# Performance work log

Measured on AMD Instinct MI355X. Metric: run time of the kernel, lower is better.

Reference implementation:

```python
import jax, jax.numpy as jnp
import numpy as np

HIDDEN_DIM = 64
VOCAB_SIZE = 128
NUM_SLOTS = 64
B, L = 256, 4096


def layer_norm(x, gamma, beta, eps=1e-5):
    mu = jnp.mean(x, axis=-1, keepdims=True)
    var = jnp.mean(jnp.square(x - mu), axis=-1, keepdims=True)
    return (x - mu) * jax.lax.rsqrt(var + eps) * gamma + beta


def _l2norm(x, axis=-1, eps=1e-12):
    # matches torch F.normalize: x / max(||x||, eps)
    n = jnp.sqrt(jnp.sum(jnp.square(x), axis=axis, keepdims=True))
    return x / jnp.maximum(n, eps)


def setup_inputs() -> dict:
    key = jax.random.key(0)
    ks = jax.random.split(key, 13)
    H, V, S = HIDDEN_DIM, VOCAB_SIZE, NUM_SLOTS
    return {
        "seq": jax.random.randint(ks[0], (B, L), 0, V),
        "embed_w": jax.random.normal(ks[1], (V, H), dtype=jnp.float32),
        # linear weights stored [in, out] (transposed vs torch)
        "w1": jax.random.normal(ks[2], (H, 2 * H), dtype=jnp.float32) * 0.05,
        "b1": jnp.zeros((2 * H,), dtype=jnp.float32),
        "w2": jax.random.normal(ks[3], (2 * H, H), dtype=jnp.float32) * 0.05,
        "b2": jnp.zeros((H,), dtype=jnp.float32),
        "ln_g": jnp.ones((H,), dtype=jnp.float32),
        "ln_b": jnp.zeros((H,), dtype=jnp.float32),
        "slot_keys": jax.random.normal(ks[4], (S, H), dtype=jnp.float32) * 0.1,
        "slot_vals": jax.random.normal(ks[5], (S, H), dtype=jnp.float32) * 0.1,
        "gate_w": jax.random.normal(ks[6], (H, S), dtype=jnp.float32) * 0.05,
        "gate_b": jnp.zeros((S,), dtype=jnp.float32),
        "out_w": jax.random.normal(ks[7], (H, V), dtype=jnp.float32) * 0.05,
        "out_b": jnp.zeros((V,), dtype=jnp.float32),
    }


def reference(seq, embed_w, w1, b1, w2, b2, ln_g, ln_b,
              slot_keys, slot_vals, gate_w, gate_b, out_w, out_b):
    h = embed_w[seq]                                   # [B, L, H]
    ff = jnp.maximum(h @ w1 + b1, 0.0) @ w2 + b2       # [B, L, H]
    h = layer_norm(h + ff, ln_g, ln_b)

    hw = h[:, :-1, :]                                  # written tokens [B, L-1, H]
    w = jax.nn.softmax(hw @ gate_w + gate_b, axis=-1)  # [B, L-1, S]
    # the per-step increment w_t (outer) h_t is independent of prior keys,
    # so the sequential loop collapses exactly to one contraction:
    keys = slot_keys[None, :, :] + jnp.einsum('btn,bth->bnh', w, hw)  # [B, S, H]
    vals = keys  # loop sets vals = keys every step; L > 1 here

    q = h[:, -1, :]                                    # [B, H]
    sim = jnp.einsum('bnh,bh->bn', _l2norm(keys), _l2norm(q))
    attn = jax.nn.softmax(sim, axis=-1)                # [B, S]
    ctx = jnp.einsum('bn,bnh->bh', attn, vals)         # [B, H]
    return ctx @ out_w + out_b                         # [B, V]
```

## Files before the change

### kernel.cpp

```cpp
#include <hip/hip_runtime.h>

#define HD 64
#define VC 128
#define NS 64
#define NB 256
#define SL 4096

__device__ __forceinline__ float wsum(float x) {
#pragma unroll
  for (int o = 32; o > 0; o >>= 1) x += __shfl_xor(x, o, 64);
  return x;
}
__device__ __forceinline__ float wmax(float x) {
#pragma unroll
  for (int o = 32; o > 0; o >>= 1) x = fmaxf(x, __shfl_xor(x, o, 64));
  return x;
}

__global__ __launch_bounds__(128) void build_tables(
    const float* __restrict__ embed, const float* __restrict__ w1, const float* __restrict__ b1,
    const float* __restrict__ w2, const float* __restrict__ b2,
    const float* __restrict__ ln_g, const float* __restrict__ ln_b,
    const float* __restrict__ gate_w, const float* __restrict__ gate_b,
    float* __restrict__ HN, float* __restrict__ WSM)
{
  const int v = blockIdx.x, t = threadIdx.x;
  __shared__ float s_e[HD], s_f1[2 * HD], s_hn[HD];

  if (t < HD) s_e[t] = embed[v * HD + t];
  __syncthreads();

  float acc = b1[t];
#pragma unroll 8
  for (int h = 0; h < HD; ++h)
    acc = fmaf(s_e[h], w1[h * 2 * HD + t], acc);
  s_f1[t] = fmaxf(acc, 0.f);
  __syncthreads();

  if (t < HD) {
    float a2 = b2[t];
#pragma unroll 8
    for (int j = 0; j < 2 * HD; ++j)
      a2 = fmaf(s_f1[j], w2[j * HD + t], a2);
    float x = s_e[t] + a2;
    float mu = wsum(x) * (1.f / 64.f);
    float d = x - mu;
    float var = wsum(d * d) * (1.f / 64.f);
    float hn = d * rsqrtf(var + 1e-5f) * ln_g[t] + ln_b[t];
    s_hn[t] = hn;
    HN[v * HD + t] = hn;
  }
  __syncthreads();

  if (t < NS) {
    float g = gate_b[t];
#pragma unroll 8
    for (int h = 0; h < HD; ++h)
      g = fmaf(s_hn[h], gate_w[h * NS + t], g);
    float m = wmax(g);
    float e = expf(g - m);
    float s = wsum(e);
    WSM[v * NS + t] = e / s;
  }
}

__global__ __launch_bounds__(512) void batch_kernel(
    const int* __restrict__ seq, const float* __restrict__ HN, const float* __restrict__ WSM,
    const float* __restrict__ slot_keys, const float* __restrict__ out_w,
    const float* __restrict__ out_b, float* __restrict__ out)
{
  const int b = blockIdx.x, t = threadIdx.x;
  const int lane = t & 63, wave = t >> 6;

  __shared__ int s_cnt[VC];
  __shared__ int s_qtok;
  __align__(16) __shared__ float s_hn[VC * HD];
  __align__(16) __shared__ float s_wsm[VC * NS];
  __align__(16) __shared__ float s_keys[NS * HD];
  __shared__ float s_part[8 * HD];
  __shared__ float s_q[HD], s_sim[NS], s_attn[NS], s_ctx[HD];

  if (t < VC) s_cnt[t] = 0;
  __syncthreads();

  const int* sb = seq + b * SL;
  for (int i = t; i < SL - 1; i += 512) atomicAdd(&s_cnt[sb[i]], 1);
  if (t == 0) s_qtok = sb[SL - 1];
#pragma unroll
  for (int i4 = t; i4 < VC * HD / 4; i4 += 512)
    ((float4*)s_hn)[i4] = ((const float4*)HN)[i4];
  __syncthreads();

  if (t < HD) s_q[t] = s_hn[s_qtok * HD + t];
#pragma unroll
  for (int i4 = t; i4 < VC * NS / 4; i4 += 512) {
    float4 wv = ((const float4*)WSM)[i4];
    const float c = (float)s_cnt[i4 >> 4];
    wv.x *= c; wv.y *= c; wv.z *= c; wv.w *= c;
    ((float4*)s_wsm)[i4] = wv;
  }
  __syncthreads();

  const int tid = t & 255;
  const int half = t >> 8;
  const int n0 = (tid >> 4) << 2;
  const int h0 = (tid & 15) << 2;
  const float* hbase = s_hn + half * 64 * HD;
  const float* wbase = s_wsm + half * 64 * NS;

  float accv[4][4];
  if (half == 0) {
#pragma unroll
    for (int r = 0; r < 4; ++r) {
      const float4 sk = *(const float4*)&slot_keys[(n0 + r) * HD + h0];
      accv[r][0] = sk.x; accv[r][1] = sk.y; accv[r][2] = sk.z; accv[r][3] = sk.w;
    }
  } else {
#pragma unroll
    for (int r = 0; r < 4; ++r)
#pragma unroll
      for (int c = 0; c < 4; ++c) accv[r][c] = 0.f;
  }

#pragma unroll 4
  for (int v = 0; v < 64; ++v) {
    const float4 hv = *(const float4*)&hbase[v * HD + h0];
    const float4 wv = *(const float4*)&wbase[v * NS + n0];
    accv[0][0] = fmaf(wv.x, hv.x, accv[0][0]);
    accv[0][1] = fmaf(wv.x, hv.y, accv[0][1]);
    accv[0][2] = fmaf(wv.x, hv.z, accv[0][2]);
    accv[0][3] = fmaf(wv.x, hv.w, accv[0][3]);
    accv[1][0] = fmaf(wv.y, hv.x, accv[1][0]);
    accv[1][1] = fmaf(wv.y, hv.y, accv[1][1]);
    accv[1][2] = fmaf(wv.y, hv.z, accv[1][2]);
    accv[1][3] = fmaf(wv.y, hv.w, accv[1][3]);
    accv[2][0] = fmaf(wv.z, hv.x, accv[2][0]);
    accv[2][1] = fmaf(wv.z, hv.y, accv[2][1]);
    accv[2][2] = fmaf(wv.z, hv.z, accv[2][2]);
    accv[2][3] = fmaf(wv.z, hv.w, accv[2][3]);
    accv[3][0] = fmaf(wv.w, hv.x, accv[3][0]);
    accv[3][1] = fmaf(wv.w, hv.y, accv[3][1]);
    accv[3][2] = fmaf(wv.w, hv.z, accv[3][2]);
    accv[3][3] = fmaf(wv.w, hv.w, accv[3][3]);
  }
  __syncthreads();

  if (half == 1) {
#pragma unroll
    for (int r = 0; r < 4; ++r) {
      float4 st; st.x = accv[r][0]; st.y = accv[r][1]; st.z = accv[r][2]; st.w = accv[r][3];
      *(float4*)&s_keys[(n0 + r) * HD + h0] = st;
    }
  }
  __syncthreads();
  if (half == 0) {
#pragma unroll
    for (int r = 0; r < 4; ++r) {
      float4 p = *(const float4*)&s_keys[(n0 + r) * HD + h0];
      p.x += accv[r][0]; p.y += accv[r][1]; p.z += accv[r][2]; p.w += accv[r][3];
      *(float4*)&s_keys[(n0 + r) * HD + h0] = p;
    }
  }
  __syncthreads();

  const float qv = s_q[lane];
  const float qn = fmaxf(sqrtf(wsum(qv * qv)), 1e-12f);
#pragma unroll
  for (int r = 0; r < 8; ++r) {
    const int n = wave * 8 + r;
    const float kv = s_keys[n * HD + lane];
    const float kk = wsum(kv * kv);
    const float kq = wsum(kv * qv);
    if (lane == 0) s_sim[n] = kq / (fmaxf(sqrtf(kk), 1e-12f) * qn);
  }
  __syncthreads();

  if (wave == 0) {
    float sv = s_sim[lane];
    float m = wmax(sv);
    float e = expf(sv - m);
    float ssum = wsum(e);
    s_attn[lane] = e / ssum;
  }
  __syncthreads();

  {
    float c = 0.f;
#pragma unroll
    for (int r = 0; r < 8; ++r) {
      const int n = wave * 8 + r;
      c = fmaf(s_attn[n], s_keys[n * HD + lane], c);
    }
    s_part[wave * HD + lane] = c;
  }
  __syncthreads();
  if (wave == 0) {
    float c = 0.f;
#pragma unroll
    for (int w = 0; w < 8; ++w) c += s_part[w * HD + lane];
    s_ctx[lane] = c;
  }
  __syncthreads();

  if (t < VC) {
    float o = out_b[t];
#pragma unroll 8
    for (int h = 0; h < HD; ++h)
      o = fmaf(s_ctx[h], out_w[h * VC + t], o);
    out[b * VC + t] = o;
  }
}

extern "C" void kernel_launch(void* const* d_in, const int* in_sizes, int n_in,
                              void* d_out, int out_size, void* d_ws, size_t ws_size,
                              hipStream_t stream) {
  const int* seq         = (const int*)d_in[0];
  const float* embed_w   = (const float*)d_in[1];
  const float* w1        = (const float*)d_in[2];
  const float* b1        = (const float*)d_in[3];
  const float* w2        = (const float*)d_in[4];
  const float* b2        = (const float*)d_in[5];
  const float* ln_g      = (const float*)d_in[6];
  const float* ln_b      = (const float*)d_in[7];
  const float* slot_keys = (const float*)d_in[8];
  const float* gate_w    = (const float*)d_in[10];
  const float* gate_b    = (const float*)d_in[11];
  const float* out_w     = (const float*)d_in[12];
  const float* out_b     = (const float*)d_in[13];
  float* out = (float*)d_out;

  float* HN  = (float*)d_ws;
  float* WSM = HN + VC * HD;

  build_tables<<<VC, 128, 0, stream>>>(embed_w, w1, b1, w2, b2, ln_g, ln_b,
                                       gate_w, gate_b, HN, WSM);
  batch_kernel<<<NB, 512, 0, stream>>>(seq, HN, WSM, slot_keys, out_w, out_b, out);
}
```

Baseline: 105.0 us.

## Use 1024-thread blocks with four-way split-K key accumulation and vectorized loads

Doubles the batch kernel's block size to 1024 threads. Each thread now does one int4 seq load and two float4 loads each for HN and WSM, replacing the strided loops, and the vocab reduction is split four ways with pairwise partial sums reusing s_hn as scratch. The aim is more memory-level parallelism and shorter per-thread serial work in the load and contraction phases. In exchange, the 1024-thread block with about 100KB of LDS limits occupancy to one block per CU and adds an extra reduction pass and barrier.

```diff
diff --git a/kernel.cpp b/kernel.cpp
--- a/kernel.cpp
+++ b/kernel.cpp
@@ -64,7 +64,7 @@
   }
 }
 
-__global__ __launch_bounds__(512) void batch_kernel(
+__global__ __launch_bounds__(1024) void batch_kernel(
     const int* __restrict__ seq, const float* __restrict__ HN, const float* __restrict__ WSM,
     const float* __restrict__ slot_keys, const float* __restrict__ out_w,
     const float* __restrict__ out_b, float* __restrict__ out)
@@ -77,39 +77,51 @@
   __align__(16) __shared__ float s_hn[VC * HD];
   __align__(16) __shared__ float s_wsm[VC * NS];
   __align__(16) __shared__ float s_keys[NS * HD];
-  __shared__ float s_part[8 * HD];
+  __align__(16) __shared__ float s_part[16 * HD];
   __shared__ float s_q[HD], s_sim[NS], s_attn[NS], s_ctx[HD];
 
   if (t < VC) s_cnt[t] = 0;
   __syncthreads();
 
   const int* sb = seq + b * SL;
-  for (int i = t; i < SL - 1; i += 512) atomicAdd(&s_cnt[sb[i]], 1);
-  if (t == 0) s_qtok = sb[SL - 1];
-#pragma unroll
-  for (int i4 = t; i4 < VC * HD / 4; i4 += 512)
-    ((float4*)s_hn)[i4] = ((const float4*)HN)[i4];
+  const int4 sv = ((const int4*)sb)[t];
+  const float4 h0v = ((const float4*)HN)[t];
+  const float4 h1v = ((const float4*)HN)[t + 1024];
+  const float4 g0v = ((const float4*)WSM)[t];
+  const float4 g1v = ((const float4*)WSM)[t + 1024];
+  atomicAdd(&s_cnt[sv.x], 1);
+  atomicAdd(&s_cnt[sv.y], 1);
+  atomicAdd(&s_cnt[sv.z], 1);
+  if (t != 1023) atomicAdd(&s_cnt[sv.w], 1);
+  else s_qtok = sv.w;
+  ((float4*)s_hn)[t] = h0v;
+  ((float4*)s_hn)[t + 1024] = h1v;
+  ((float4*)s_wsm)[t] = g0v;
+  ((float4*)s_wsm)[t + 1024] = g1v;
   __syncthreads();
 
   if (t < HD) s_q[t] = s_hn[s_qtok * HD + t];
-#pragma unroll
-  for (int i4 = t; i4 < VC * NS / 4; i4 += 512) {
-    float4 wv = ((const float4*)WSM)[i4];
-    const float c = (float)s_cnt[i4 >> 4];
-    wv.x *= c; wv.y *= c; wv.z *= c; wv.w *= c;
-    ((float4*)s_wsm)[i4] = wv;
-  }
-  __syncthreads();
-
+  {
+    float4 a = ((const float4*)s_wsm)[t];
+    float4 c = ((const float4*)s_wsm)[t + 1024];
+    const float c0 = (float)s_cnt[t >> 4];
+    const float c1 = (float)s_cnt[(t + 1024) >> 4];
+    a.x *= c0; a.y *= c0; a.z *= c0; a.w *= c0;
+    c.x *= c1; c.y *= c1; c.z *= c1; c.w *= c1;
+    ((float4*)s_wsm)[t] = a;
+    ((float4*)s_wsm)[t + 1024] = c;
+  }
+  __syncthreads();
+
+  const int qt = t >> 8;
   const int tid = t & 255;
-  const int half = t >> 8;
   const int n0 = (tid >> 4) << 2;
   const int h0 = (tid & 15) << 2;
-  const float* hbase = s_hn + half * 64 * HD;
-  const float* wbase = s_wsm + half * 64 * NS;
+  const float* hb = s_hn + qt * 32 * HD;
+  const float* wb = s_wsm + qt * 32 * NS;
 
   float accv[4][4];
-  if (half == 0) {
+  if (qt == 0) {
 #pragma unroll
     for (int r = 0; r < 4; ++r) {
       const float4 sk = *(const float4*)&slot_keys[(n0 + r) * HD + h0];
@@ -123,9 +135,9 @@
   }
 
 #pragma unroll 4
-  for (int v = 0; v < 64; ++v) {
-    const float4 hv = *(const float4*)&hbase[v * HD + h0];
-    const float4 wv = *(const float4*)&wbase[v * NS + n0];
+  for (int v = 0; v < 32; ++v) {
+    const float4 hv = *(const float4*)&hb[v * HD + h0];
+    const float4 wv = *(const float4*)&wb[v * NS + n0];
     accv[0][0] = fmaf(wv.x, hv.x, accv[0][0]);
     accv[0][1] = fmaf(wv.x, hv.y, accv[0][1]);
     accv[0][2] = fmaf(wv.x, hv.z, accv[0][2]);
@@ -145,29 +157,51 @@
   }
   __syncthreads();
 
-  if (half == 1) {
+  float* kA = s_hn;
+  float* kB = s_hn + NS * HD;
+  if (qt == 1) {
 #pragma unroll
     for (int r = 0; r < 4; ++r) {
       float4 st; st.x = accv[r][0]; st.y = accv[r][1]; st.z = accv[r][2]; st.w = accv[r][3];
-      *(float4*)&s_keys[(n0 + r) * HD + h0] = st;
-    }
-  }
-  __syncthreads();
-  if (half == 0) {
-#pragma unroll
-    for (int r = 0; r < 4; ++r) {
-      float4 p = *(const float4*)&s_keys[(n0 + r) * HD + h0];
+      *(float4*)&kA[(n0 + r) * HD + h0] = st;
+    }
+  } else if (qt == 3) {
+#pragma unroll
+    for (int r = 0; r < 4; ++r) {
+      float4 st; st.x = accv[r][0]; st.y = accv[r][1]; st.z = accv[r][2]; st.w = accv[r][3];
+      *(float4*)&kB[(n0 + r) * HD + h0] = st;
+    }
+  }
+  __syncthreads();
+  if (qt == 0) {
+#pragma unroll
+    for (int r = 0; r < 4; ++r) {
+      float4 p = *(const float4*)&kA[(n0 + r) * HD + h0];
       p.x += accv[r][0]; p.y += accv[r][1]; p.z += accv[r][2]; p.w += accv[r][3];
-      *(float4*)&s_keys[(n0 + r) * HD + h0] = p;
-    }
+      *(float4*)&kA[(n0 + r) * HD + h0] = p;
+    }
+  } else if (qt == 2) {
+#pragma unroll
+    for (int r = 0; r < 4; ++r) {
+      float4 p = *(const float4*)&kB[(n0 + r) * HD + h0];
+      p.x += accv[r][0]; p.y += accv[r][1]; p.z += accv[r][2]; p.w += accv[r][3];
+      *(float4*)&kB[(n0 + r) * HD + h0] = p;
+    }
+  }
+  __syncthreads();
+  {
+    float4 a = ((const float4*)kA)[t];
+    const float4 c = ((const float4*)kB)[t];
+    a.x += c.x; a.y += c.y; a.z += c.z; a.w += c.w;
+    ((float4*)s_keys)[t] = a;
   }
   __syncthreads();
 
   const float qv = s_q[lane];
   const float qn = fmaxf(sqrtf(wsum(qv * qv)), 1e-12f);
 #pragma unroll
-  for (int r = 0; r < 8; ++r) {
-    const int n = wave * 8 + r;
+  for (int r = 0; r < 4; ++r) {
+    const int n = (wave << 2) + r;
     const float kv = s_keys[n * HD + lane];
     const float kk = wsum(kv * kv);
     const float kq = wsum(kv * qv);
@@ -176,9 +210,9 @@
   __syncthreads();
 
   if (wave == 0) {
-    float sv = s_sim[lane];
-    float m = wmax(sv);
-    float e = expf(sv - m);
+    float svv = s_sim[lane];
+    float m = wmax(svv);
+    float e = expf(svv - m);
     float ssum = wsum(e);
     s_attn[lane] = e / ssum;
   }
@@ -187,8 +221,8 @@
   {
     float c = 0.f;
 #pragma unroll
-    for (int r = 0; r < 8; ++r) {
-      const int n = wave * 8 + r;
+    for (int r = 0; r < 4; ++r) {
+      const int n = (wave << 2) + r;
       c = fmaf(s_attn[n], s_keys[n * HD + lane], c);
     }
     s_part[wave * HD + lane] = c;
@@ -197,7 +231,7 @@
   if (wave == 0) {
     float c = 0.f;
 #pragma unroll
-    for (int w = 0; w < 8; ++w) c += s_part[w * HD + lane];
+    for (int w = 0; w < 16; ++w) c += s_part[w * HD + lane];
     s_ctx[lane] = c;
   }
   __syncthreads();
@@ -234,5 +268,5 @@
 
   build_tables<<<VC, 128, 0, stream>>>(embed_w, w1, b1, w2, b2, ln_g, ln_b,
                                        gate_w, gate_b, HN, WSM);
-  batch_kernel<<<NB, 512, 0, stream>>>(seq, HN, WSM, slot_keys, out_w, out_b, out);
-}
+  batch_kernel<<<NB, 1024, 0, stream>>>(seq, HN, WSM, slot_keys, out_w, out_b, out);
+}
```

Measured after the change: 101.7 us. 1.03x faster.
